# Kernel tuning notes

Hardware: AMD Instinct MI355X
Metric: run time of the kernel (lower is better)

Reference implementation:

```python
import jax, jax.numpy as jnp
import numpy as np

N = 400000
H = 256          # hidden_dim
NUM_HEADS = 4
HEAD_DIM = H // NUM_HEADS
B = 1024         # number of graphs (segments)


def setup_inputs() -> dict:
    key = jax.random.key(0)
    ks = jax.random.split(key, 6)
    x = jax.random.normal(ks[0], (N, H), dtype=jnp.float32)
    batch = jnp.sort(jax.random.randint(ks[1], (N,), 0, B, dtype=jnp.int64))
    s = 1.0 / np.sqrt(H)
    W1 = jax.random.normal(ks[2], (H, H), dtype=jnp.float32) * s
    b1 = jnp.zeros((H,), dtype=jnp.float32)
    W2 = jax.random.normal(ks[3], (H, NUM_HEADS), dtype=jnp.float32) * s
    b2 = jnp.zeros((NUM_HEADS,), dtype=jnp.float32)
    Wt = jax.random.normal(ks[4], (H, H), dtype=jnp.float32) * s
    bt = jnp.zeros((H,), dtype=jnp.float32)
    return {"x": x, "batch": batch, "W1": W1, "b1": b1, "W2": W2, "b2": b2, "Wt": Wt, "bt": bt}


def reference(x, batch, W1, b1, W2, b2, Wt, bt):
    # attention MLP: Linear -> Tanh -> Linear  -> [N, num_heads]
    logits = jnp.tanh(x @ W1 + b1) @ W2 + b2
    # segment (per-graph) softmax over nodes, per head (PyG-style with 1e-16 eps)
    seg_max = jax.ops.segment_max(logits, batch, num_segments=B)        # [B, heads]
    e = jnp.exp(logits - seg_max[batch])                                # [N, heads]
    seg_sum = jax.ops.segment_sum(e, batch, num_segments=B)             # [B, heads]
    attn = e / (seg_sum[batch] + 1e-16)                                 # [N, heads]
    # transform + per-head weighting
    xt = (x @ Wt + bt).reshape(N, NUM_HEADS, HEAD_DIM)
    weighted = (attn[:, :, None] * xt).reshape(N, H)
    # global add pool over each graph
    graph_emb = jax.ops.segment_sum(weighted, batch, num_segments=B)    # [B, hidden]
    return graph_emb, attn
```

## Files before the change

kernel.cpp:

```cpp
#include <hip/hip_runtime.h>
#include <math.h>

#define HD    256
#define NHEAD 4
#define NSEG  1024

typedef short bf16x8 __attribute__((ext_vector_type(8)));
typedef float f32x16 __attribute__((ext_vector_type(16)));

__device__ __forceinline__ float tanh_fast(float v) {
    float e = __expf(2.0f * v);
    return 1.0f - 2.0f * __builtin_amdgcn_rcpf(e + 1.0f);
}

__device__ __forceinline__ void split2(float a, float b, unsigned &hi, unsigned &lo) {
    unsigned ba = __float_as_uint(a), bb = __float_as_uint(b);
    unsigned ha = ba & 0xFFFF0000u, hb = bb & 0xFFFF0000u;
    float la = a - __uint_as_float(ha);
    float lb = b - __uint_as_float(hb);
    hi = (ha >> 16) | hb;
    lo = (__float_as_uint(la) >> 16) | (__float_as_uint(lb) & 0xFFFF0000u);
}

__device__ __forceinline__ void gld16(const void* g, void* l) {
    __builtin_amdgcn_global_load_lds(
        (const __attribute__((address_space(1))) void*)g,
        (__attribute__((address_space(3))) void*)l, 16, 0, 0);
}

__global__ __launch_bounds__(256) void k0_prep(
    const float* __restrict__ W1, char* __restrict__ ws)
{
    int g = blockIdx.x * 256 + threadIdx.x;
    int c  = g & 255;
    int j  = (g >> 8) & 3;
    int h  = (g >> 10) & 3;
    int t  = g >> 12;
    int k  = t*32 + h*8 + 2*j;
    float a = W1[(size_t)k * HD + c];
    float b = W1[(size_t)(k + 1) * HD + c];
    unsigned hw, lw;
    split2(a, b, hw, lw);
    size_t off = (size_t)t*32768 + h*4096 + c*16 + j*4;
    *(unsigned*)(ws + off)         = hw;
    *(unsigned*)(ws + off + 16384) = lw;
}

#define K1_THREADS 512
#define BM 256
#define KC 32
#define NCHUNK (HD/KC)
#define BUFB 65536
#define K1_LDS (2*BUFB)

__global__ __launch_bounds__(K1_THREADS, 2) void k1_mfma(
    const float* __restrict__ x, const char* __restrict__ wsW,
    const float* __restrict__ b1, const float* __restrict__ W2,
    const float* __restrict__ b2, float* __restrict__ out_lg, int N)
{
    extern __shared__ __align__(16) char smem[];

    const int tid  = threadIdx.x;
    const int lane = tid & 63;
    const int lo5  = lane & 31;
    const int hi   = lane >> 5;
    const int wid  = tid >> 6;
    const int rg   = wid >> 1;
    const int cg   = wid & 1;
    const int C0   = cg * 128;
    const int blkrow = blockIdx.x * BM;

    f32x16 acc[2][4];
    #pragma unroll
    for (int ct = 0; ct < 4; ++ct) {
        float b1v = b1[C0 + ct*32 + lo5];
        #pragma unroll
        for (int rt = 0; rt < 2; ++rt)
            #pragma unroll
            for (int e = 0; e < 16; ++e)
                acc[rt][ct][e] = b1v;
    }

    const char* gx[4];
    #pragma unroll
    for (int i = 0; i < 4; ++i) {
        int p    = i*8192 + tid*16;
        int row  = p >> 7;
        int slot = (p >> 4) & 7;
        long grow = blkrow + row; if (grow > N-1) grow = N-1;
        gx[i] = (const char*)x + grow*1024 + ((slot ^ (row & 7)) * 16);
    }
    const char* gw[4];
    #pragma unroll
    for (int j = 0; j < 4; ++j)
        gw[j] = wsW + j*8192 + tid*16;

    #pragma unroll
    for (int i = 0; i < 4; ++i) gld16(gx[i], smem + i*8192 + tid*16);
    #pragma unroll
    for (int j = 0; j < 4; ++j) gld16(gw[j], smem + 32768 + j*8192 + tid*16);
    __syncthreads();

    for (int t = 0; t < NCHUNK; ++t) {
        const int buf  = (t & 1) * BUFB;
        const int nbuf = BUFB - buf;
        if (t < NCHUNK-1) {
            #pragma unroll
            for (int i = 0; i < 4; ++i)
                gld16(gx[i] + (size_t)(t+1)*128, smem + nbuf + i*8192 + tid*16);
            #pragma unroll
            for (int j = 0; j < 4; ++j)
                gld16(gw[j] + (size_t)(t+1)*32768, smem + nbuf + 32768 + j*8192 + tid*16);
        }
        #pragma unroll
        for (int ks = 0; ks < 2; ++ks) {
            union { unsigned u[4]; bf16x8 v; } ah[2], al[2];
            #pragma unroll
            for (int rt = 0; rt < 2; ++rt) {
                int rl = rg*64 + rt*32 + lo5;
                int base = buf + rl*128;
                int s0 = (ks*4 + hi*2)     ^ (rl & 7);
                int s1 = (ks*4 + hi*2 + 1) ^ (rl & 7);
                float4 q0 = *(const float4*)(smem + base + s0*16);
                float4 q1 = *(const float4*)(smem + base + s1*16);
                split2(q0.x, q0.y, ah[rt].u[0], al[rt].u[0]);
                split2(q0.z, q0.w, ah[rt].u[1], al[rt].u[1]);
                split2(q1.x, q1.y, ah[rt].u[2], al[rt].u[2]);
                split2(q1.z, q1.w, ah[rt].u[3], al[rt].u[3]);
            }
            bf16x8 bh[4], bl[4];
            #pragma unroll
            for (int ct = 0; ct < 4; ++ct) {
                int col = C0 + ct*32 + lo5;
                int off = buf + 32768 + (ks*2 + hi)*4096 + col*16;
                bh[ct] = *(const bf16x8*)(smem + off);
                bl[ct] = *(const bf16x8*)(smem + off + 16384);
            }
            #pragma unroll
            for (int rt = 0; rt < 2; ++rt)
                #pragma unroll
                for (int ct = 0; ct < 4; ++ct) {
                    acc[rt][ct] = __builtin_amdgcn_mfma_f32_32x32x16_bf16(ah[rt].v, bh[ct], acc[rt][ct], 0, 0, 0);
                    acc[rt][ct] = __builtin_amdgcn_mfma_f32_32x32x16_bf16(ah[rt].v, bl[ct], acc[rt][ct], 0, 0, 0);
                    acc[rt][ct] = __builtin_amdgcn_mfma_f32_32x32x16_bf16(al[rt].v, bh[ct], acc[rt][ct], 0, 0, 0);
                }
        }
        __syncthreads();
    }

    #pragma unroll
    for (int rt = 0; rt < 2; ++rt)
        #pragma unroll
        for (int ct = 0; ct < 4; ++ct)
            #pragma unroll
            for (int e = 0; e < 16; ++e)
                acc[rt][ct][e] = tanh_fast(acc[rt][ct][e]);

    float4 w2v[4];
    #pragma unroll
    for (int ct = 0; ct < 4; ++ct)
        w2v[ct] = *(const float4*)(W2 + (size_t)(C0 + ct*32 + lo5) * NHEAD);

    float4 mine = make_float4(0.f, 0.f, 0.f, 0.f);
    #pragma unroll
    for (int rt = 0; rt < 2; ++rt) {
        #pragma unroll
        for (int e = 0; e < 16; ++e) {
            float s0 = 0.f, s1 = 0.f, s2 = 0.f, s3 = 0.f;
            #pragma unroll
            for (int ct = 0; ct < 4; ++ct) {
                float tv = acc[rt][ct][e];
                s0 = fmaf(tv, w2v[ct].x, s0);
                s1 = fmaf(tv, w2v[ct].y, s1);
                s2 = fmaf(tv, w2v[ct].z, s2);
                s3 = fmaf(tv, w2v[ct].w, s3);
            }
            #pragma unroll
            for (int o = 16; o >= 1; o >>= 1) {
                s0 += __shfl_xor(s0, o, 64);
                s1 += __shfl_xor(s1, o, 64);
                s2 += __shfl_xor(s2, o, 64);
                s3 += __shfl_xor(s3, o, 64);
            }
            if (lo5 == rt*16 + e) mine = make_float4(s0, s1, s2, s3);
        }
    }
    const int e_m = lo5 & 15, rt_m = lo5 >> 4;
    const int myrow = rg*64 + rt_m*32 + (e_m & 3) + 8*(e_m >> 2) + 4*hi;

    __syncthreads();
    float (*p_lds)[256][4] = (float(*)[256][4])smem;
    *(float4*)p_lds[cg][myrow] = mine;
    __syncthreads();
    if (tid < BM) {
        int grow = blkrow + tid;
        if (grow < N) {
            float4 a0 = *(float4*)p_lds[0][tid];
            float4 a1 = *(float4*)p_lds[1][tid];
            float4 o;
            o.x = a0.x + a1.x + b2[0];
            o.y = a0.y + a1.y + b2[1];
            o.z = a0.z + a1.z + b2[2];
            o.w = a0.w + a1.w + b2[3];
            *(float4*)(out_lg + (size_t)grow * NHEAD) = o;
        }
    }
}

__device__ __forceinline__ int lower_bound(const int* __restrict__ a, int n, int v) {
    int lo = 0, hi = n;
    while (lo < hi) { int m = (lo + hi) >> 1; if (a[m] < v) lo = m + 1; else hi = m; }
    return lo;
}

__global__ __launch_bounds__(256) void k2_seg(
    const int* __restrict__ batch, const float* __restrict__ lg,
    float* __restrict__ out, int N)
{
    const int b = blockIdx.x;
    const int tid = threadIdx.x;
    const int lane = tid & 63, wid = tid >> 6;
    const int start = lower_bound(batch, N, b);
    const int end   = lower_bound(batch, N, b + 1);
    const float4* lg4 = (const float4*)lg;

    float4 mx = make_float4(-INFINITY, -INFINITY, -INFINITY, -INFINITY);
    for (int i = start + tid; i < end; i += 256) {
        float4 l = lg4[i];
        mx.x = fmaxf(mx.x, l.x); mx.y = fmaxf(mx.y, l.y);
        mx.z = fmaxf(mx.z, l.z); mx.w = fmaxf(mx.w, l.w);
    }
    #pragma unroll
    for (int ofs = 32; ofs >= 1; ofs >>= 1) {
        mx.x = fmaxf(mx.x, __shfl_xor(mx.x, ofs, 64));
        mx.y = fmaxf(mx.y, __shfl_xor(mx.y, ofs, 64));
        mx.z = fmaxf(mx.z, __shfl_xor(mx.z, ofs, 64));
        mx.w = fmaxf(mx.w, __shfl_xor(mx.w, ofs, 64));
    }
    __shared__ float4 red[4];
    if (lane == 0) red[wid] = mx;
    __syncthreads();
    float4 smax;
    smax.x = fmaxf(fmaxf(red[0].x, red[1].x), fmaxf(red[2].x, red[3].x));
    smax.y = fmaxf(fmaxf(red[0].y, red[1].y), fmaxf(red[2].y, red[3].y));
    smax.z = fmaxf(fmaxf(red[0].z, red[1].z), fmaxf(red[2].z, red[3].z));
    smax.w = fmaxf(fmaxf(red[0].w, red[1].w), fmaxf(red[2].w, red[3].w));
    __syncthreads();

    float4 sm = make_float4(0.f, 0.f, 0.f, 0.f);
    for (int i = start + tid; i < end; i += 256) {
        float4 l = lg4[i];
        sm.x += __expf(l.x - smax.x); sm.y += __expf(l.y - smax.y);
        sm.z += __expf(l.z - smax.z); sm.w += __expf(l.w - smax.w);
    }
    #pragma unroll
    for (int ofs = 32; ofs >= 1; ofs >>= 1) {
        sm.x += __shfl_xor(sm.x, ofs, 64);
        sm.y += __shfl_xor(sm.y, ofs, 64);
        sm.z += __shfl_xor(sm.z, ofs, 64);
        sm.w += __shfl_xor(sm.w, ofs, 64);
    }
    if (lane == 0) red[wid] = sm;
    __syncthreads();
    if (tid == 0) {
        float4 ssum;
        ssum.x = red[0].x + red[1].x + red[2].x + red[3].x;
        ssum.y = red[0].y + red[1].y + red[2].y + red[3].y;
        ssum.z = red[0].z + red[1].z + red[2].z + red[3].z;
        ssum.w = red[0].w + red[1].w + red[2].w + red[3].w;
        *(float4*)(out + (size_t)b * HD)     = smax;
        *(float4*)(out + (size_t)b * HD + 4) = ssum;
    }
}

__global__ __launch_bounds__(256) void k3_pool(
    const int* __restrict__ batch, const float* __restrict__ x,
    const float* __restrict__ Wt, const float* __restrict__ bt,
    float* __restrict__ out, int N)
{
    const int b = blockIdx.x;
    const int tid = threadIdx.x;
    const int start = lower_bound(batch, N, b);
    const int end   = lower_bound(batch, N, b + 1);

    float4* at4 = (float4*)(out + (size_t)NSEG * HD);

    const float4 smax = *(const float4*)(out + (size_t)b * HD);
    const float4 ssum = *(const float4*)(out + (size_t)b * HD + 4);
    float4 inv;
    inv.x = 1.0f / (ssum.x + 1e-16f); inv.y = 1.0f / (ssum.y + 1e-16f);
    inv.z = 1.0f / (ssum.z + 1e-16f); inv.w = 1.0f / (ssum.w + 1e-16f);

    float z0 = 0.f, z1 = 0.f, z2 = 0.f, z3 = 0.f;
    __shared__ float4 attn_s[256];

    for (int c0 = start; c0 < end; c0 += 256) {
        const int idx = c0 + tid;
        if (idx < end) {
            float4 l = at4[idx];
            float4 a;
            a.x = __expf(l.x - smax.x) * inv.x;
            a.y = __expf(l.y - smax.y) * inv.y;
            a.z = __expf(l.z - smax.z) * inv.z;
            a.w = __expf(l.w - smax.w) * inv.w;
            at4[idx] = a;
            attn_s[tid] = a;
        }
        __syncthreads();
        const int cnt = min(256, end - c0);
        const float* xb = x + (size_t)c0 * HD + tid;
        #pragma unroll 4
        for (int i = 0; i < cnt; ++i) {
            float4 a = attn_s[i];
            float xv = xb[(size_t)i * HD];
            z0 = fmaf(a.x, xv, z0); z1 = fmaf(a.y, xv, z1);
            z2 = fmaf(a.z, xv, z2); z3 = fmaf(a.w, xv, z3);
        }
        __syncthreads();
    }

    __shared__ float zs[NHEAD][HD];
    zs[0][tid] = z0; zs[1][tid] = z1; zs[2][tid] = z2; zs[3][tid] = z3;
    __syncthreads();

    const int h = tid >> 6;
    float smh, invh;
    if      (h == 0) { smh = ssum.x; invh = inv.x; }
    else if (h == 1) { smh = ssum.y; invh = inv.y; }
    else if (h == 2) { smh = ssum.z; invh = inv.z; }
    else             { smh = ssum.w; invh = inv.w; }

    float acc = smh * invh * bt[tid];
    #pragma unroll 4
    for (int k = 0; k < HD; ++k)
        acc = fmaf(zs[h][k], Wt[(size_t)k * HD + tid], acc);

    out[(size_t)b * HD + tid] = acc;
}

extern "C" void kernel_launch(void* const* d_in, const int* in_sizes, int n_in,
                              void* d_out, int out_size, void* d_ws, size_t ws_size,
                              hipStream_t stream) {
    const float* x   = (const float*)d_in[0];
    const int*   bat = (const int*)  d_in[1];
    const float* W1  = (const float*)d_in[2];
    const float* b1  = (const float*)d_in[3];
    const float* W2  = (const float*)d_in[4];
    const float* b2  = (const float*)d_in[5];
    const float* Wt  = (const float*)d_in[6];
    const float* bt  = (const float*)d_in[7];
    float* out = (float*)d_out;
    const int N = in_sizes[0] / HD;

    float* out_lg = out + (size_t)NSEG * HD;

    hipLaunchKernelGGL(k0_prep, dim3(128), dim3(256), 0, stream, W1, (char*)d_ws);
    hipLaunchKernelGGL(k1_mfma, dim3((N + BM - 1) / BM), dim3(K1_THREADS),
                       K1_LDS, stream, x, (const char*)d_ws, b1, W2, b2, out_lg, N);
    hipLaunchKernelGGL(k2_seg, dim3(NSEG), dim3(256), 0, stream, bat, out_lg, out, N);
    hipLaunchKernelGGL(k3_pool, dim3(NSEG), dim3(256), 0, stream, bat, x, Wt, bt, out, N);
}
```

Baseline: 393.3 us.

## Split logits GEMM across column halves with direct x loads and partial logits

The attention MLP kernel now splits the 256 hidden columns into two halves handled by separate 256-thread blocks over 128-row tiles. Blocks for the same rows are interleaved so the repeated x reads can hit in L2. x is read straight from global memory into registers instead of being staged through LDS, which shrinks LDS use so more blocks fit per CU. Each half writes its own partial logits (lgA and lgB), and the softmax and pooling kernels sum the two. The cost is reading x twice, extra global traffic for the second logits buffer, and uncoalesced per-lane row loads of x.

```diff
diff --git a/kernel.cpp b/kernel.cpp
--- a/kernel.cpp
+++ b/kernel.cpp
@@ -4,6 +4,7 @@
 #define HD    256
 #define NHEAD 4
 #define NSEG  1024
+#define NRB   3125
 
 typedef short bf16x8 __attribute__((ext_vector_type(8)));
 typedef float f32x16 __attribute__((ext_vector_type(16)));
@@ -32,33 +33,37 @@
     const float* __restrict__ W1, char* __restrict__ ws)
 {
     int g = blockIdx.x * 256 + threadIdx.x;
-    int c  = g & 255;
-    int j  = (g >> 8) & 3;
-    int h  = (g >> 10) & 3;
+    int c  = g & 127;
+    int j  = (g >> 7) & 3;
+    int o  = (g >> 9) & 3;
+    int ch = (g >> 11) & 1;
     int t  = g >> 12;
-    int k  = t*32 + h*8 + 2*j;
-    float a = W1[(size_t)k * HD + c];
-    float b = W1[(size_t)(k + 1) * HD + c];
+    int k   = t*32 + o*8 + 2*j;
+    int col = ch*128 + c;
+    float a = W1[(size_t)k * HD + col];
+    float b = W1[(size_t)(k + 1) * HD + col];
     unsigned hw, lw;
     split2(a, b, hw, lw);
-    size_t off = (size_t)t*32768 + h*4096 + c*16 + j*4;
-    *(unsigned*)(ws + off)         = hw;
-    *(unsigned*)(ws + off + 16384) = lw;
-}
-
-#define K1_THREADS 512
-#define BM 256
-#define KC 32
-#define NCHUNK (HD/KC)
-#define BUFB 65536
-#define K1_LDS (2*BUFB)
-
-__global__ __launch_bounds__(K1_THREADS, 2) void k1_mfma(
+    size_t off = (size_t)t*32768 + ch*16384 + o*2048 + c*16 + j*4;
+    *(unsigned*)(ws + off)        = hw;
+    *(unsigned*)(ws + off + 8192) = lw;
+}
+
+#define K1_THREADS 256
+#define K1_LDS 32768
+
+__global__ __launch_bounds__(K1_THREADS, 3) void k1_mfma(
     const float* __restrict__ x, const char* __restrict__ wsW,
     const float* __restrict__ b1, const float* __restrict__ W2,
-    const float* __restrict__ b2, float* __restrict__ out_lg, int N)
+    const float* __restrict__ b2, float* __restrict__ lgA,
+    float* __restrict__ lgB, int N)
 {
     extern __shared__ __align__(16) char smem[];
+
+    const int raw = blockIdx.x;
+    const int ch  = (raw >> 3) & 1;
+    const int rb  = (raw >> 4) * 8 + (raw & 7);
+    if (rb >= NRB) return;
 
     const int tid  = threadIdx.x;
     const int lane = tid & 63;
@@ -67,13 +72,12 @@
     const int wid  = tid >> 6;
     const int rg   = wid >> 1;
     const int cg   = wid & 1;
-    const int C0   = cg * 128;
-    const int blkrow = blockIdx.x * BM;
-
-    f32x16 acc[2][4];
-    #pragma unroll
-    for (int ct = 0; ct < 4; ++ct) {
-        float b1v = b1[C0 + ct*32 + lo5];
+    const int blkrow = rb * 128;
+
+    f32x16 acc[2][2];
+    #pragma unroll
+    for (int ct = 0; ct < 2; ++ct) {
+        float b1v = b1[ch*128 + cg*64 + ct*32 + lo5];
         #pragma unroll
         for (int rt = 0; rt < 2; ++rt)
             #pragma unroll
@@ -81,65 +85,50 @@
                 acc[rt][ct][e] = b1v;
     }
 
-    const char* gx[4];
-    #pragma unroll
-    for (int i = 0; i < 4; ++i) {
-        int p    = i*8192 + tid*16;
-        int row  = p >> 7;
-        int slot = (p >> 4) & 7;
-        long grow = blkrow + row; if (grow > N-1) grow = N-1;
-        gx[i] = (const char*)x + grow*1024 + ((slot ^ (row & 7)) * 16);
-    }
-    const char* gw[4];
-    #pragma unroll
-    for (int j = 0; j < 4; ++j)
-        gw[j] = wsW + j*8192 + tid*16;
-
-    #pragma unroll
-    for (int i = 0; i < 4; ++i) gld16(gx[i], smem + i*8192 + tid*16);
-    #pragma unroll
-    for (int j = 0; j < 4; ++j) gld16(gw[j], smem + 32768 + j*8192 + tid*16);
-    __syncthreads();
-
-    for (int t = 0; t < NCHUNK; ++t) {
-        const int buf  = (t & 1) * BUFB;
-        const int nbuf = BUFB - buf;
-        if (t < NCHUNK-1) {
+    int rA[2];
+    #pragma unroll
+    for (int rt = 0; rt < 2; ++rt) {
+        int r = blkrow + rg*64 + rt*32 + lo5;
+        rA[rt] = r < N ? r : N - 1;
+    }
+
+    const char* gw = wsW + ch*16384 + tid*16;
+    #pragma unroll
+    for (int i = 0; i < 4; ++i) gld16(gw + i*4096, smem + i*4096 + tid*16);
+    __syncthreads();
+
+    for (int t = 0; t < 8; ++t) {
+        const int buf = (t & 1) * 16384;
+        if (t < 7) {
+            const char* src = gw + (size_t)(t+1)*32768;
             #pragma unroll
             for (int i = 0; i < 4; ++i)
-                gld16(gx[i] + (size_t)(t+1)*128, smem + nbuf + i*8192 + tid*16);
-            #pragma unroll
-            for (int j = 0; j < 4; ++j)
-                gld16(gw[j] + (size_t)(t+1)*32768, smem + nbuf + 32768 + j*8192 + tid*16);
+                gld16(src + i*4096, smem + (buf ^ 16384) + i*4096 + tid*16);
         }
         #pragma unroll
         for (int ks = 0; ks < 2; ++ks) {
             union { unsigned u[4]; bf16x8 v; } ah[2], al[2];
             #pragma unroll
             for (int rt = 0; rt < 2; ++rt) {
-                int rl = rg*64 + rt*32 + lo5;
-                int base = buf + rl*128;
-                int s0 = (ks*4 + hi*2)     ^ (rl & 7);
-                int s1 = (ks*4 + hi*2 + 1) ^ (rl & 7);
-                float4 q0 = *(const float4*)(smem + base + s0*16);
-                float4 q1 = *(const float4*)(smem + base + s1*16);
+                const float* xp = x + (size_t)rA[rt]*HD + t*32 + ks*16 + hi*8;
+                float4 q0 = *(const float4*)xp;
+                float4 q1 = *(const float4*)(xp + 4);
                 split2(q0.x, q0.y, ah[rt].u[0], al[rt].u[0]);
                 split2(q0.z, q0.w, ah[rt].u[1], al[rt].u[1]);
                 split2(q1.x, q1.y, ah[rt].u[2], al[rt].u[2]);
                 split2(q1.z, q1.w, ah[rt].u[3], al[rt].u[3]);
             }
-            bf16x8 bh[4], bl[4];
-            #pragma unroll
-            for (int ct = 0; ct < 4; ++ct) {
-                int col = C0 + ct*32 + lo5;
-                int off = buf + 32768 + (ks*2 + hi)*4096 + col*16;
+            bf16x8 bh[2], bl[2];
+            #pragma unroll
+            for (int ct = 0; ct < 2; ++ct) {
+                int off = buf + (ks*2 + hi)*2048 + (cg*64 + ct*32 + lo5)*16;
                 bh[ct] = *(const bf16x8*)(smem + off);
-                bl[ct] = *(const bf16x8*)(smem + off + 16384);
+                bl[ct] = *(const bf16x8*)(smem + off + 8192);
             }
             #pragma unroll
             for (int rt = 0; rt < 2; ++rt)
                 #pragma unroll
-                for (int ct = 0; ct < 4; ++ct) {
+                for (int ct = 0; ct < 2; ++ct) {
                     acc[rt][ct] = __builtin_amdgcn_mfma_f32_32x32x16_bf16(ah[rt].v, bh[ct], acc[rt][ct], 0, 0, 0);
                     acc[rt][ct] = __builtin_amdgcn_mfma_f32_32x32x16_bf16(ah[rt].v, bl[ct], acc[rt][ct], 0, 0, 0);
                     acc[rt][ct] = __builtin_amdgcn_mfma_f32_32x32x16_bf16(al[rt].v, bh[ct], acc[rt][ct], 0, 0, 0);
@@ -151,15 +140,15 @@
     #pragma unroll
     for (int rt = 0; rt < 2; ++rt)
         #pragma unroll
-        for (int ct = 0; ct < 4; ++ct)
+        for (int ct = 0; ct < 2; ++ct)
             #pragma unroll
             for (int e = 0; e < 16; ++e)
                 acc[rt][ct][e] = tanh_fast(acc[rt][ct][e]);
 
-    float4 w2v[4];
-    #pragma unroll
-    for (int ct = 0; ct < 4; ++ct)
-        w2v[ct] = *(const float4*)(W2 + (size_t)(C0 + ct*32 + lo5) * NHEAD);
+    float4 w2v[2];
+    #pragma unroll
+    for (int ct = 0; ct < 2; ++ct)
+        w2v[ct] = *(const float4*)(W2 + (size_t)(ch*128 + cg*64 + ct*32 + lo5) * NHEAD);
 
     float4 mine = make_float4(0.f, 0.f, 0.f, 0.f);
     #pragma unroll
@@ -168,7 +157,7 @@
         for (int e = 0; e < 16; ++e) {
             float s0 = 0.f, s1 = 0.f, s2 = 0.f, s3 = 0.f;
             #pragma unroll
-            for (int ct = 0; ct < 4; ++ct) {
+            for (int ct = 0; ct < 2; ++ct) {
                 float tv = acc[rt][ct][e];
                 s0 = fmaf(tv, w2v[ct].x, s0);
                 s1 = fmaf(tv, w2v[ct].y, s1);
@@ -188,21 +177,23 @@
     const int e_m = lo5 & 15, rt_m = lo5 >> 4;
     const int myrow = rg*64 + rt_m*32 + (e_m & 3) + 8*(e_m >> 2) + 4*hi;
 
-    __syncthreads();
-    float (*p_lds)[256][4] = (float(*)[256][4])smem;
+    float (*p_lds)[128][4] = (float(*)[128][4])smem;
     *(float4*)p_lds[cg][myrow] = mine;
     __syncthreads();
-    if (tid < BM) {
+    if (tid < 128) {
         int grow = blkrow + tid;
         if (grow < N) {
             float4 a0 = *(float4*)p_lds[0][tid];
             float4 a1 = *(float4*)p_lds[1][tid];
             float4 o;
-            o.x = a0.x + a1.x + b2[0];
-            o.y = a0.y + a1.y + b2[1];
-            o.z = a0.z + a1.z + b2[2];
-            o.w = a0.w + a1.w + b2[3];
-            *(float4*)(out_lg + (size_t)grow * NHEAD) = o;
+            o.x = a0.x + a1.x; o.y = a0.y + a1.y;
+            o.z = a0.z + a1.z; o.w = a0.w + a1.w;
+            float* dst;
+            if (ch == 0) {
+                o.x += b2[0]; o.y += b2[1]; o.z += b2[2]; o.w += b2[3];
+                dst = lgA;
+            } else dst = lgB;
+            *(float4*)(dst + (size_t)grow * NHEAD) = o;
         }
     }
 }
@@ -214,21 +205,22 @@
 }
 
 __global__ __launch_bounds__(256) void k2_seg(
-    const int* __restrict__ batch, const float* __restrict__ lg,
-    float* __restrict__ out, int N)
+    const int* __restrict__ batch, const float* __restrict__ lgA,
+    const float* __restrict__ lgB, float* __restrict__ out, int N)
 {
     const int b = blockIdx.x;
     const int tid = threadIdx.x;
     const int lane = tid & 63, wid = tid >> 6;
     const int start = lower_bound(batch, N, b);
     const int end   = lower_bound(batch, N, b + 1);
-    const float4* lg4 = (const float4*)lg;
+    const float4* la4 = (const float4*)lgA;
+    const float4* lb4 = (const float4*)lgB;
 
     float4 mx = make_float4(-INFINITY, -INFINITY, -INFINITY, -INFINITY);
     for (int i = start + tid; i < end; i += 256) {
-        float4 l = lg4[i];
-        mx.x = fmaxf(mx.x, l.x); mx.y = fmaxf(mx.y, l.y);
-        mx.z = fmaxf(mx.z, l.z); mx.w = fmaxf(mx.w, l.w);
+        float4 a = la4[i], bq = lb4[i];
+        mx.x = fmaxf(mx.x, a.x + bq.x); mx.y = fmaxf(mx.y, a.y + bq.y);
+        mx.z = fmaxf(mx.z, a.z + bq.z); mx.w = fmaxf(mx.w, a.w + bq.w);
     }
     #pragma unroll
     for (int ofs = 32; ofs >= 1; ofs >>= 1) {
@@ -249,9 +241,9 @@
 
     float4 sm = make_float4(0.f, 0.f, 0.f, 0.f);
     for (int i = start + tid; i < end; i += 256) {
-        float4 l = lg4[i];
-        sm.x += __expf(l.x - smax.x); sm.y += __expf(l.y - smax.y);
-        sm.z += __expf(l.z - smax.z); sm.w += __expf(l.w - smax.w);
+        float4 a = la4[i], bq = lb4[i];
+        sm.x += __expf(a.x + bq.x - smax.x); sm.y += __expf(a.y + bq.y - smax.y);
+        sm.z += __expf(a.z + bq.z - smax.z); sm.w += __expf(a.w + bq.w - smax.w);
     }
     #pragma unroll
     for (int ofs = 32; ofs >= 1; ofs >>= 1) {
@@ -276,7 +268,7 @@
 __global__ __launch_bounds__(256) void k3_pool(
     const int* __restrict__ batch, const float* __restrict__ x,
     const float* __restrict__ Wt, const float* __restrict__ bt,
-    float* __restrict__ out, int N)
+    const float* __restrict__ lgB, float* __restrict__ out, int N)
 {
     const int b = blockIdx.x;
     const int tid = threadIdx.x;
@@ -284,6 +276,7 @@
     const int end   = lower_bound(batch, N, b + 1);
 
     float4* at4 = (float4*)(out + (size_t)NSEG * HD);
+    const float4* lb4 = (const float4*)lgB;
 
     const float4 smax = *(const float4*)(out + (size_t)b * HD);
     const float4 ssum = *(const float4*)(out + (size_t)b * HD + 4);
@@ -298,11 +291,12 @@
         const int idx = c0 + tid;
         if (idx < end) {
             float4 l = at4[idx];
+            float4 lb = lb4[idx];
             float4 a;
-            a.x = __expf(l.x - smax.x) * inv.x;
-            a.y = __expf(l.y - smax.y) * inv.y;
-            a.z = __expf(l.z - smax.z) * inv.z;
-            a.w = __expf(l.w - smax.w) * inv.w;
+            a.x = __expf(l.x + lb.x - smax.x) * inv.x;
+            a.y = __expf(l.y + lb.y - smax.y) * inv.y;
+            a.z = __expf(l.z + lb.z - smax.z) * inv.z;
+            a.w = __expf(l.w + lb.w - smax.w) * inv.w;
             at4[idx] = a;
             attn_s[tid] = a;
         }
@@ -352,11 +346,13 @@
     float* out = (float*)d_out;
     const int N = in_sizes[0] / HD;
 
-    float* out_lg = out + (size_t)NSEG * HD;
-
-    hipLaunchKernelGGL(k0_prep, dim3(128), dim3(256), 0, stream, W1, (char*)d_ws);
-    hipLaunchKernelGGL(k1_mfma, dim3((N + BM - 1) / BM), dim3(K1_THREADS),
-                       K1_LDS, stream, x, (const char*)d_ws, b1, W2, b2, out_lg, N);
-    hipLaunchKernelGGL(k2_seg, dim3(NSEG), dim3(256), 0, stream, bat, out_lg, out, N);
-    hipLaunchKernelGGL(k3_pool, dim3(NSEG), dim3(256), 0, stream, bat, x, Wt, bt, out, N);
-}
+    float* lgA = out + (size_t)NSEG * HD;
+    char*  wsW = (char*)d_ws;
+    float* lgB = (float*)((char*)d_ws + 262144);
+
+    hipLaunchKernelGGL(k0_prep, dim3(128), dim3(256), 0, stream, W1, wsW);
+    hipLaunchKernelGGL(k1_mfma, dim3(((NRB + 7) / 8) * 16), dim3(K1_THREADS),
+                       K1_LDS, stream, x, wsW, b1, W2, b2, lgA, lgB, N);
+    hipLaunchKernelGGL(k2_seg, dim3(NSEG), dim3(256), 0, stream, bat, lgA, lgB, out, N);
+    hipLaunchKernelGGL(k3_pool, dim3(NSEG), dim3(256), 0, stream, bat, x, Wt, bt, lgB, out, N);
+}
```

New measurement: 424.2 us. 7.9% more time.
